# Optimization experiments

Measured on AMD Instinct MI355X. Metric: run time of the kernel, lower is better.

The kernel has to match this reference:

```python
import jax, jax.numpy as jnp
import numpy as np

N_NODES = 50000
N_EDGES = 640000
IN_C, HID_C, OUT_C = 64, 128, 64


def _glorot(key, fan_in, fan_out):
    lim = float(np.sqrt(6.0 / (fan_in + fan_out)))
    return jax.random.uniform(key, (fan_in, fan_out), jnp.float32, -lim, lim)


def setup_inputs() -> dict:
    key = jax.random.key(0)
    ks = jax.random.split(key, 16)
    x = jax.random.normal(ks[0], (N_NODES, IN_C), jnp.float32)
    edge_index = jax.random.randint(ks[1], (2, N_EDGES), 0, N_NODES, jnp.int64)
    # SAGEConv params: out = mean_aggr(x_j) @ Wl + x @ Wr + b
    dims = [(IN_C, HID_C), (HID_C, HID_C), (HID_C, OUT_C)]
    params = {}
    for i, (fi, fo) in enumerate(dims):
        params[f"Wl{i}"] = _glorot(ks[2 + 3 * i], fi, fo)
        params[f"Wr{i}"] = _glorot(ks[3 + 3 * i], fi, fo)
        params[f"b{i}"] = jnp.zeros((fo,), jnp.float32)
    # classifier: Linear(64,32) -> ReLU -> Linear(32,1) -> Sigmoid (dropout off in eval)
    params["Wc1"] = _glorot(ks[11], OUT_C, 32)
    params["bc1"] = jnp.zeros((32,), jnp.float32)
    params["Wc2"] = _glorot(ks[12], 32, 1)
    params["bc2"] = jnp.zeros((1,), jnp.float32)
    return {"x": x, "edge_index": edge_index, **params}


def _sage_conv(x, src, dst, Wl, Wr, b):
    # gather neighbor (source) features along edges, mean-aggregate at target
    msgs = x[src]                                                    # [E, C]
    agg = jax.ops.segment_sum(msgs, dst, num_segments=N_NODES)      # [N, C]
    deg = jax.ops.segment_sum(jnp.ones((src.shape[0], 1), x.dtype), dst,
                              num_segments=N_NODES)                 # [N, 1]
    agg = agg / jnp.maximum(deg, 1.0)
    return agg @ Wl + x @ Wr + b


def reference(x, edge_index, Wl0, Wr0, b0, Wl1, Wr1, b1, Wl2, Wr2, b2,
              Wc1, bc1, Wc2, bc2):
    src, dst = edge_index[0], edge_index[1]
    h = jax.nn.relu(_sage_conv(x, src, dst, Wl0, Wr0, b0))
    h = jax.nn.relu(_sage_conv(h, src, dst, Wl1, Wr1, b1))
    h = _sage_conv(h, src, dst, Wl2, Wr2, b2)                       # [N, 64]
    h = jax.nn.relu(h @ Wc1 + bc1)                                  # [N, 32]
    return jax.nn.sigmoid(h @ Wc2 + bc2)                            # [N, 1]
```

## Files before the change

kernel.cpp:

```cpp
#include <hip/hip_runtime.h>
#include <hip/hip_cooperative_groups.h>
#include <math.h>

namespace cg = cooperative_groups;

#define NN 50000
#define NE 640000
#define CAP 64

typedef short short8 __attribute__((ext_vector_type(8)));
typedef float f32x4  __attribute__((ext_vector_type(4)));

__device__ __forceinline__ unsigned bfr(float f) {
    unsigned u = __float_as_uint(f);
    return (u + 0x7FFFu + ((u >> 16) & 1u)) >> 16;
}
__device__ __forceinline__ unsigned pk2(float a, float b) { return bfr(a) | (bfr(b) << 16); }
__device__ __forceinline__ float bflo(unsigned u) { return __uint_as_float(u << 16); }
__device__ __forceinline__ float bfhi(unsigned u) { return __uint_as_float(u & 0xFFFF0000u); }

__device__ __forceinline__ void packOne(const float* Wl, const float* Wr,
                                        unsigned short* wp, int idx,
                                        int CIN, int COUT) {
    int k = idx / COUT, n = idx % COUT;
    float v = (k < CIN) ? Wl[k * COUT + n] : Wr[(k - CIN) * COUT + n];
    int kt = k >> 5, quad = (k >> 3) & 3, j = k & 7;
    int nt = n >> 4, l16 = n & 15;
    int NT = COUT / 16;
    wp[(((kt * NT + nt) * 64) + quad * 16 + l16) * 8 + j] = (unsigned short)bfr(v);
}

template <int LOGC>
__device__ __forceinline__ void
agg_phase(const unsigned* __restrict__ xu, const int* __restrict__ nbr,
          const int* __restrict__ cnt, unsigned* __restrict__ aggu,
          int gid, int ngroups, int l16) {
    constexpr int RU = 1 << (LOGC - 1);
    constexpr int PC = RU / 16;

    for (int gw = gid; gw < NN; gw += ngroups) {
        const int deg = cnt[gw];
        const int m = (deg < CAP) ? deg : CAP;

        float a[2 * PC] = {};

        for (int base = 0; base < m; base += 16) {
            int idx = NN;
            if (base + l16 < m) idx = nbr[gw * CAP + base + l16];
#pragma unroll
            for (int j = 0; j < 16; ++j) {
                const int n = __shfl(idx, j, 16);
                if (PC == 2) {
                    const uint2 u = *(const uint2*)(xu + (size_t)n * RU + l16 * 2);
                    a[0] += bflo(u.x); a[1] += bfhi(u.x);
                    a[2] += bflo(u.y); a[3] += bfhi(u.y);
                } else {
                    const uint4 u = *(const uint4*)(xu + (size_t)n * RU + l16 * 4);
                    a[0] += bflo(u.x); a[1] += bfhi(u.x);
                    a[2] += bflo(u.y); a[3] += bfhi(u.y);
                    a[4] += bflo(u.z); a[5] += bfhi(u.z);
                    a[6] += bflo(u.w); a[7] += bfhi(u.w);
                }
            }
        }

        const float di = 1.0f / (float)((deg > 1) ? deg : 1);
        if (PC == 2) {
            uint2 o = make_uint2(pk2(a[0] * di, a[1] * di), pk2(a[2] * di, a[3] * di));
            *(uint2*)(aggu + (size_t)gw * RU + l16 * 2) = o;
        } else {
            uint4 o = make_uint4(pk2(a[0] * di, a[1] * di), pk2(a[2] * di, a[3] * di),
                                 pk2(a[4] * di, a[5] * di), pk2(a[6] * di, a[7] * di));
            *(uint4*)(aggu + (size_t)gw * RU + l16 * 4) = o;
        }
    }
}

template <int CIN, int COUT, bool RELU>
__device__ __forceinline__ void
mfma_phase(const unsigned short* __restrict__ Agg, const unsigned short* __restrict__ X,
           const unsigned short* __restrict__ Wpack, const float* __restrict__ bias,
           unsigned short* __restrict__ outp, int blk, int gstride, int wave, int lane) {
    constexpr int KT = (2 * CIN) / 32;
    constexpr int NT = COUT / 16;
    const int quad = lane >> 4, l16 = lane & 15;
    const int NTILE = (NN + 127) / 128;

    for (int tile = blk; tile < NTILE; tile += gstride) {
        const int row_base = tile * 128 + wave * 32;
        int r0 = row_base + l16;      if (r0 >= NN) r0 = NN - 1;
        int r1 = row_base + 16 + l16; if (r1 >= NN) r1 = NN - 1;

        f32x4 acc[2][NT] = {};

        for (int kt = 0; kt < KT; ++kt) {
            const unsigned short* P = (kt < KT / 2) ? Agg : X;
            const int kb = (kt < KT / 2) ? kt * 32 : kt * 32 - CIN;
            const short8 a0 = *(const short8*)(P + (size_t)r0 * CIN + kb + quad * 8);
            const short8 a1 = *(const short8*)(P + (size_t)r1 * CIN + kb + quad * 8);
#pragma unroll
            for (int nt = 0; nt < NT; ++nt) {
                const short8 bfrag = *(const short8*)(Wpack + (size_t)((kt * NT + nt) * 64 + lane) * 8);
                acc[0][nt] = __builtin_amdgcn_mfma_f32_16x16x32_bf16(a0, bfrag, acc[0][nt], 0, 0, 0);
                acc[1][nt] = __builtin_amdgcn_mfma_f32_16x16x32_bf16(a1, bfrag, acc[1][nt], 0, 0, 0);
            }
        }

#pragma unroll
        for (int nt = 0; nt < NT; ++nt) {
            const int col = nt * 16 + l16;
            const float bb = bias[col];
#pragma unroll
            for (int s = 0; s < 2; ++s) {
#pragma unroll
                for (int rg = 0; rg < 4; ++rg) {
                    int row = row_base + s * 16 + quad * 4 + rg;
                    if (row < NN) {
                        float v = acc[s][nt][rg] + bb;
                        if (RELU) v = fmaxf(v, 0.f);
                        outp[(size_t)row * COUT + col] = (unsigned short)bfr(v);
                    }
                }
            }
        }
    }
}

__global__ __launch_bounds__(256) void
k_all(const int* __restrict__ src, const int* __restrict__ dst,
      const float* __restrict__ x,
      const float* Wl0, const float* Wr0, const float* b0,
      const float* Wl1, const float* Wr1, const float* b1,
      const float* Wl2, const float* Wr2, const float* b2,
      const float* Wc1, const float* bc1, const float* Wc2, const float* bc2,
      int* cnt, int* nbr, unsigned short* xb,
      unsigned short* wp0, unsigned short* wp1, unsigned short* wp2,
      unsigned short* wpc,
      unsigned short* aggb, unsigned short* h0b, unsigned short* h1b,
      float* out) {
    cg::grid_group grid = cg::this_grid();

    __shared__ __align__(16) short Hs[8 * 16 * 64];

    const int t = threadIdx.x, b = blockIdx.x;
    const int nthr = gridDim.x * 256;
    const int gt = b * 256 + t;
    const int wave = t >> 6, lane = t & 63;
    const int quad = lane >> 4, l16 = lane & 15;
    const int gid = gt >> 4;
    const int ngroups = nthr >> 4;

    for (int e = gt; e < NE; e += nthr) {
        int d = dst[e];
        int p = atomicAdd(&cnt[d], 1);
        if (p < CAP) nbr[d * CAP + p] = src[e];
    }
    for (int i = gt; i < NN * 16; i += nthr) {
        float4 v = ((const float4*)x)[i];
        ((uint2*)xb)[i] = make_uint2(pk2(v.x, v.y), pk2(v.z, v.w));
    }
    if (gt < 32) ((unsigned*)xb)[(size_t)NN * 32 + gt] = 0u;
    else if (gt < 96) ((unsigned*)h0b)[(size_t)NN * 64 + (gt - 32)] = 0u;
    else if (gt < 160) ((unsigned*)h1b)[(size_t)NN * 64 + (gt - 96)] = 0u;
    for (int i = gt; i < 67584; i += nthr) {
        if (i < 16384) packOne(Wl0, Wr0, wp0, i, 64, 128);
        else if (i < 49152) packOne(Wl1, Wr1, wp1, i - 16384, 128, 128);
        else if (i < 65536) packOne(Wl2, Wr2, wp2, i - 49152, 128, 64);
        else packOne(Wc1, Wc1, wpc, i - 65536, 64, 32);
    }
    grid.sync();

    agg_phase<6>((const unsigned*)xb, nbr, cnt, (unsigned*)aggb, gid, ngroups, t & 15);
    grid.sync();
    mfma_phase<64, 128, true>(aggb, xb, wp0, b0, h0b, b, gridDim.x, wave, lane);
    grid.sync();

    agg_phase<7>((const unsigned*)h0b, nbr, cnt, (unsigned*)aggb, gid, ngroups, t & 15);
    grid.sync();
    mfma_phase<128, 128, true>(aggb, h0b, wp1, b1, h1b, b, gridDim.x, wave, lane);
    grid.sync();

    agg_phase<7>((const unsigned*)h1b, nbr, cnt, (unsigned*)aggb, gid, ngroups, t & 15);
    grid.sync();

    {
        constexpr int CIN = 128, NT = 4, KT = 8;
        const int NTILE = (NN + 127) / 128;

        for (int tile = b; tile < NTILE; tile += gridDim.x) {
            const int row_base = tile * 128 + wave * 32;
            int r0 = row_base + l16;      if (r0 >= NN) r0 = NN - 1;
            int r1 = row_base + 16 + l16; if (r1 >= NN) r1 = NN - 1;

            f32x4 acc[2][NT] = {};

            for (int kt = 0; kt < KT; ++kt) {
                const unsigned short* P = (kt < KT / 2) ? aggb : h1b;
                const int kb = (kt < KT / 2) ? kt * 32 : kt * 32 - CIN;
                const short8 a0 = *(const short8*)(P + (size_t)r0 * CIN + kb + quad * 8);
                const short8 a1 = *(const short8*)(P + (size_t)r1 * CIN + kb + quad * 8);
#pragma unroll
                for (int nt = 0; nt < NT; ++nt) {
                    const short8 bfrag = *(const short8*)(wp2 + (size_t)((kt * NT + nt) * 64 + lane) * 8);
                    acc[0][nt] = __builtin_amdgcn_mfma_f32_16x16x32_bf16(a0, bfrag, acc[0][nt], 0, 0, 0);
                    acc[1][nt] = __builtin_amdgcn_mfma_f32_16x16x32_bf16(a1, bfrag, acc[1][nt], 0, 0, 0);
                }
            }

#pragma unroll
            for (int nt = 0; nt < NT; ++nt) {
                const float bb = b2[nt * 16 + l16];
#pragma unroll
                for (int s = 0; s < 2; ++s)
#pragma unroll
                    for (int rg = 0; rg < 4; ++rg)
                        Hs[(wave * 2 + s) * 1024 + (quad * 4 + rg) * 64 + nt * 16 + l16] =
                            (unsigned short)bfr(acc[s][nt][rg] + bb);
            }
            __syncthreads();

            f32x4 sacc[2][2] = {};
#pragma unroll
            for (int s = 0; s < 2; ++s)
#pragma unroll
                for (int kt2 = 0; kt2 < 2; ++kt2) {
                    const short8 af = *(const short8*)&Hs[(wave * 2 + s) * 1024 + l16 * 64 +
                                                          kt2 * 32 + quad * 8];
#pragma unroll
                    for (int nt2 = 0; nt2 < 2; ++nt2) {
                        const short8 bf = *(const short8*)(wpc + (size_t)((kt2 * 2 + nt2) * 64 + lane) * 8);
                        sacc[s][nt2] = __builtin_amdgcn_mfma_f32_16x16x32_bf16(af, bf, sacc[s][nt2], 0, 0, 0);
                    }
                }

            const float b1a = bc1[l16], b1b = bc1[16 + l16];
            const float w2a = Wc2[l16], w2b = Wc2[16 + l16];
            const float b2v = bc2[0];
#pragma unroll
            for (int s = 0; s < 2; ++s)
#pragma unroll
                for (int rg = 0; rg < 4; ++rg) {
                    float p = fmaxf(sacc[s][0][rg] + b1a, 0.f) * w2a +
                              fmaxf(sacc[s][1][rg] + b1b, 0.f) * w2b;
#pragma unroll
                    for (int off = 1; off < 16; off <<= 1) p += __shfl_xor(p, off);
                    if (l16 == 0) {
                        int row = row_base + s * 16 + quad * 4 + rg;
                        if (row < NN) out[row] = 1.0f / (1.0f + expf(-(p + b2v)));
                    }
                }
            __syncthreads();
        }
    }
}

__global__ __launch_bounds__(256) void
k_prep(const int* __restrict__ src, const int* __restrict__ dst,
       int* __restrict__ cnt, int* __restrict__ nbr,
       const float* __restrict__ x, unsigned* __restrict__ xb,
       const float* Wl0, const float* Wr0, const float* Wl1, const float* Wr1,
       const float* Wl2, const float* Wr2, const float* Wc1,
       unsigned short* wp0, unsigned short* wp1, unsigned short* wp2,
       unsigned short* wpc, unsigned short* h0b, unsigned short* h1b) {
    const int b = blockIdx.x, t = threadIdx.x;
    if (b < 2500) {
        int e = b * 256 + t;
        if (e < NE) {
            int d = dst[e];
            int p = atomicAdd(&cnt[d], 1);
            if (p < CAP) nbr[d * CAP + p] = src[e];
        }
        if (b == 0) {
            if (t < 32) xb[(size_t)NN * 32 + t] = 0u;
            else if (t < 96) ((unsigned*)h0b)[(size_t)NN * 64 + (t - 32)] = 0u;
            else if (t < 160) ((unsigned*)h1b)[(size_t)NN * 64 + (t - 96)] = 0u;
        }
    } else if (b < 5625) {
        int i = (b - 2500) * 256 + t;
        if (i < NN * 16) {
            float4 v = ((const float4*)x)[i];
            ((uint2*)xb)[i] = make_uint2(pk2(v.x, v.y), pk2(v.z, v.w));
        }
    } else {
        int idx = (b - 5625) * 256 + t;
        if (idx < 16384) packOne(Wl0, Wr0, wp0, idx, 64, 128);
        else if (idx < 49152) packOne(Wl1, Wr1, wp1, idx - 16384, 128, 128);
        else if (idx < 65536) packOne(Wl2, Wr2, wp2, idx - 49152, 128, 64);
        else if (idx < 67584) packOne(Wc1, Wc1, wpc, idx - 65536, 64, 32);
    }
}

template <int LOGC>
__global__ __launch_bounds__(256) void
k_aggregate(const unsigned* __restrict__ xu, const int* __restrict__ nbr,
            const int* __restrict__ cnt, unsigned* __restrict__ aggu, int N) {
    const int gid = (blockIdx.x * 256 + threadIdx.x) >> 4;
    if (gid >= N) return;
    agg_phase<LOGC>(xu, nbr, cnt, aggu, gid, 1 << 30, threadIdx.x & 15);
}

template <int CIN, int COUT, bool RELU>
__global__ __launch_bounds__(256) void
k_mfma(const unsigned short* __restrict__ Agg, const unsigned short* __restrict__ X,
       const unsigned short* __restrict__ Wpack, const float* __restrict__ bias,
       unsigned short* __restrict__ outp, int N) {
    mfma_phase<CIN, COUT, RELU>(Agg, X, Wpack, bias, outp,
                                blockIdx.x, 1 << 30, threadIdx.x >> 6, threadIdx.x & 63);
}

__global__ __launch_bounds__(256) void
k_mfma_cls(const unsigned short* __restrict__ Agg, const unsigned short* __restrict__ X,
           const unsigned short* __restrict__ Wpack, const unsigned short* __restrict__ WpackC,
           const float* __restrict__ bias, const float* __restrict__ bc1,
           const float* __restrict__ Wc2, const float* __restrict__ bc2,
           float* __restrict__ out, int N) {
    constexpr int CIN = 128, NT = 4, KT = 8;

    __shared__ __align__(16) short Hs[8 * 16 * 64];

    const int t = threadIdx.x;
    const int wave = t >> 6, lane = t & 63;
    const int quad = lane >> 4, l16 = lane & 15;

    const int row_base = blockIdx.x * 128 + wave * 32;
    int r0 = row_base + l16;      if (r0 >= N) r0 = N - 1;
    int r1 = row_base + 16 + l16; if (r1 >= N) r1 = N - 1;

    f32x4 acc[2][NT] = {};

    for (int kt = 0; kt < KT; ++kt) {
        const unsigned short* P = (kt < KT / 2) ? Agg : X;
        const int kb = (kt < KT / 2) ? kt * 32 : kt * 32 - CIN;
        const short8 a0 = *(const short8*)(P + (size_t)r0 * CIN + kb + quad * 8);
        const short8 a1 = *(const short8*)(P + (size_t)r1 * CIN + kb + quad * 8);
#pragma unroll
        for (int nt = 0; nt < NT; ++nt) {
            const short8 bfrag = *(const short8*)(Wpack + (size_t)((kt * NT + nt) * 64 + lane) * 8);
            acc[0][nt] = __builtin_amdgcn_mfma_f32_16x16x32_bf16(a0, bfrag, acc[0][nt], 0, 0, 0);
            acc[1][nt] = __builtin_amdgcn_mfma_f32_16x16x32_bf16(a1, bfrag, acc[1][nt], 0, 0, 0);
        }
    }

#pragma unroll
    for (int nt = 0; nt < NT; ++nt) {
        const float bb = bias[nt * 16 + l16];
#pragma unroll
        for (int s = 0; s < 2; ++s)
#pragma unroll
            for (int rg = 0; rg < 4; ++rg)
                Hs[(wave * 2 + s) * 1024 + (quad * 4 + rg) * 64 + nt * 16 + l16] =
                    (unsigned short)bfr(acc[s][nt][rg] + bb);
    }
    __syncthreads();

    f32x4 sacc[2][2] = {};
#pragma unroll
    for (int s = 0; s < 2; ++s)
#pragma unroll
        for (int kt2 = 0; kt2 < 2; ++kt2) {
            const short8 af = *(const short8*)&Hs[(wave * 2 + s) * 1024 + l16 * 64 +
                                                  kt2 * 32 + quad * 8];
#pragma unroll
            for (int nt2 = 0; nt2 < 2; ++nt2) {
                const short8 bf = *(const short8*)(WpackC + (size_t)((kt2 * 2 + nt2) * 64 + lane) * 8);
                sacc[s][nt2] = __builtin_amdgcn_mfma_f32_16x16x32_bf16(af, bf, sacc[s][nt2], 0, 0, 0);
            }
        }

    const float b1a = bc1[l16], b1b = bc1[16 + l16];
    const float w2a = Wc2[l16], w2b = Wc2[16 + l16];
    const float b2v = bc2[0];
#pragma unroll
    for (int s = 0; s < 2; ++s)
#pragma unroll
        for (int rg = 0; rg < 4; ++rg) {
            float p = fmaxf(sacc[s][0][rg] + b1a, 0.f) * w2a +
                      fmaxf(sacc[s][1][rg] + b1b, 0.f) * w2b;
#pragma unroll
            for (int off = 1; off < 16; off <<= 1) p += __shfl_xor(p, off);
            if (l16 == 0) {
                int row = row_base + s * 16 + quad * 4 + rg;
                if (row < N) out[row] = 1.0f / (1.0f + expf(-(p + b2v)));
            }
        }
}

extern "C" void kernel_launch(void* const* d_in, const int* in_sizes, int n_in,
                              void* d_out, int out_size, void* d_ws, size_t ws_size,
                              hipStream_t stream) {
    const float* x   = (const float*)d_in[0];
    const int*   ei  = (const int*)d_in[1];
    const int*   src = ei;
    const int*   dst = ei + NE;
    const float* Wl0 = (const float*)d_in[2];
    const float* Wr0 = (const float*)d_in[3];
    const float* b0  = (const float*)d_in[4];
    const float* Wl1 = (const float*)d_in[5];
    const float* Wr1 = (const float*)d_in[6];
    const float* b1  = (const float*)d_in[7];
    const float* Wl2 = (const float*)d_in[8];
    const float* Wr2 = (const float*)d_in[9];
    const float* b2  = (const float*)d_in[10];
    const float* Wc1 = (const float*)d_in[11];
    const float* bc1 = (const float*)d_in[12];
    const float* Wc2 = (const float*)d_in[13];
    const float* bc2 = (const float*)d_in[14];
    float* out = (float*)d_out;

    char*  ws   = (char*)d_ws;
    int*   cnt  = (int*)(ws);
    unsigned short* wp0 = (unsigned short*)(ws + (size_t)256 * 1024);
    unsigned short* wp1 = (unsigned short*)(ws + (size_t)352 * 1024);
    unsigned short* wp2 = (unsigned short*)(ws + (size_t)448 * 1024);
    unsigned short* wpc = (unsigned short*)(ws + (size_t)512 * 1024);
    int*   nbr  = (int*)(ws + (size_t)1 * (1 << 20));
    unsigned short* xb   = (unsigned short*)(ws + (size_t)16 * (1 << 20));
    unsigned short* aggb = (unsigned short*)(ws + (size_t)24 * (1 << 20));
    unsigned short* h0b  = (unsigned short*)(ws + (size_t)40 * (1 << 20));
    unsigned short* h1b  = (unsigned short*)(ws + (size_t)56 * (1 << 20));

    hipMemsetAsync(cnt, 0, (size_t)NN * sizeof(int), stream);

    bool coop_ok = false;
    int maxBpc = 0, ncu = 0, dev = 0;
    hipGetDevice(&dev);
    hipDeviceGetAttribute(&ncu, hipDeviceAttributeMultiprocessorCount, dev);
    hipError_t qerr = hipOccupancyMaxActiveBlocksPerMultiprocessor(
        &maxBpc, (const void*)k_all, 256, 0);
    if (qerr == hipSuccess && maxBpc > 0 && ncu > 0) {
        int grid = maxBpc * ncu;
        if (grid > 2048) grid = 2048;
        const int* srcp = src; const int* dstp = dst;
        void* args[] = {
            (void*)&srcp, (void*)&dstp, (void*)&x,
            (void*)&Wl0, (void*)&Wr0, (void*)&b0,
            (void*)&Wl1, (void*)&Wr1, (void*)&b1,
            (void*)&Wl2, (void*)&Wr2, (void*)&b2,
            (void*)&Wc1, (void*)&bc1, (void*)&Wc2, (void*)&bc2,
            (void*)&cnt, (void*)&nbr, (void*)&xb,
            (void*)&wp0, (void*)&wp1, (void*)&wp2, (void*)&wpc,
            (void*)&aggb, (void*)&h0b, (void*)&h1b,
            (void*)&out
        };
        hipError_t lerr = hipLaunchCooperativeKernel((const void*)k_all, dim3(grid),
                                                     dim3(256), args, 0, stream);
        if (lerr == hipSuccess) coop_ok = true;
        else (void)hipGetLastError();
    } else {
        (void)hipGetLastError();
    }

    if (!coop_ok) {
        const int B = 256;
        const int AGG_GRID = (NN * 16 + 255) / 256;
        const int MFMA_GRID = (NN + 127) / 128;

        k_prep<<<5889, B, 0, stream>>>(src, dst, cnt, nbr, x, (unsigned*)xb,
                                       Wl0, Wr0, Wl1, Wr1, Wl2, Wr2, Wc1,
                                       wp0, wp1, wp2, wpc, h0b, h1b);

        k_aggregate<6><<<AGG_GRID, B, 0, stream>>>((const unsigned*)xb, nbr, cnt,
                                                   (unsigned*)aggb, NN);
        k_mfma<64, 128, true><<<MFMA_GRID, B, 0, stream>>>(aggb, xb, wp0, b0, h0b, NN);

        k_aggregate<7><<<AGG_GRID, B, 0, stream>>>((const unsigned*)h0b, nbr, cnt,
                                                   (unsigned*)aggb, NN);
        k_mfma<128, 128, true><<<MFMA_GRID, B, 0, stream>>>(aggb, h0b, wp1, b1, h1b, NN);

        k_aggregate<7><<<AGG_GRID, B, 0, stream>>>((const unsigned*)h1b, nbr, cnt,
                                                   (unsigned*)aggb, NN);
        k_mfma_cls<<<MFMA_GRID, B, 0, stream>>>(aggb, h1b, wp2, wpc, b2, bc1, Wc2, bc2,
                                                out, NN);
    }
}
```

Before: 239.1 us.

## Fuse neighbor aggregation with MFMA linear per tile through LDS

Each layer's mean aggregation now runs per 64-row tile, writing the averaged features into shared memory. The MFMA matmul for that tile reads them straight back, which removes the global aggb round trip and half of the grid-wide barriers. The launch bounds add a minimum of 3 blocks per SM to hold occupancy. In exchange, the aggregation and MFMA work now alternate inside each block with __syncthreads between them, and tiles shrink from 128 to 64 rows.

Measured after the change: 676.8 us. 2.83x slower.

```diff
diff --git a/kernel.cpp b/kernel.cpp
--- a/kernel.cpp
+++ b/kernel.cpp
@@ -28,6 +28,202 @@
     int nt = n >> 4, l16 = n & 15;
     int NT = COUT / 16;
     wp[(((kt * NT + nt) * 64) + quad * 16 + l16) * 8 + j] = (unsigned short)bfr(v);
+}
+
+template <int CIN, int COUT, bool RELU, bool CLS>
+__device__ __forceinline__ void
+fused_layer(const unsigned* __restrict__ Fu, const unsigned short* __restrict__ Fs,
+            const int* __restrict__ nbr, const int* __restrict__ cnt,
+            const unsigned short* __restrict__ Wpack, const float* __restrict__ bias,
+            unsigned short* __restrict__ outp,
+            const unsigned short* __restrict__ WpackC, const float* __restrict__ bc1,
+            const float* __restrict__ Wc2, const float* __restrict__ bc2,
+            float* __restrict__ outf,
+            short* __restrict__ lds, int blk, int gstride, int t) {
+    constexpr int RU = CIN / 2;
+    constexpr int PC = RU / 16;
+    constexpr int RS = CIN + 8;
+    constexpr int KT = (2 * CIN) / 32;
+    constexpr int NT = COUT / 16;
+    const int NTILE = (NN + 63) / 64;
+
+    const int g = t >> 4, lg = t & 15;
+    const int wave = t >> 6, lane = t & 63;
+    const int quad = lane >> 4, l16 = lane & 15;
+
+    for (int tile = blk; tile < NTILE; tile += gstride) {
+#pragma unroll
+        for (int i = 0; i < 4; ++i) {
+            const int rloc = g * 4 + i;
+            const int gw = tile * 64 + rloc;
+            if (gw < NN) {
+                const int deg = cnt[gw];
+                const int m = (deg < CAP) ? deg : CAP;
+                float a[2 * PC] = {};
+                for (int base = 0; base < m; base += 16) {
+                    int idx = NN;
+                    if (base + lg < m) idx = nbr[gw * CAP + base + lg];
+#pragma unroll
+                    for (int j = 0; j < 16; ++j) {
+                        const int n = __shfl(idx, j, 16);
+                        if (PC == 2) {
+                            const uint2 u = *(const uint2*)(Fu + (size_t)n * RU + lg * 2);
+                            a[0] += bflo(u.x); a[1] += bfhi(u.x);
+                            a[2] += bflo(u.y); a[3] += bfhi(u.y);
+                        } else {
+                            const uint4 u = *(const uint4*)(Fu + (size_t)n * RU + lg * 4);
+                            a[0] += bflo(u.x); a[1] += bfhi(u.x);
+                            a[2] += bflo(u.y); a[3] += bfhi(u.y);
+                            a[4] += bflo(u.z); a[5] += bfhi(u.z);
+                            a[6] += bflo(u.w); a[7] += bfhi(u.w);
+                        }
+                    }
+                }
+                const float di = 1.0f / (float)((deg > 1) ? deg : 1);
+                unsigned* lrow = (unsigned*)lds + (size_t)rloc * (RU + 4) + lg * PC;
+                if (PC == 2)
+                    *(uint2*)lrow = make_uint2(pk2(a[0] * di, a[1] * di),
+                                               pk2(a[2] * di, a[3] * di));
+                else
+                    *(uint4*)lrow = make_uint4(pk2(a[0] * di, a[1] * di),
+                                               pk2(a[2] * di, a[3] * di),
+                                               pk2(a[4] * di, a[5] * di),
+                                               pk2(a[6] * di, a[7] * di));
+            }
+        }
+        __syncthreads();
+
+        const int rbase = tile * 64 + wave * 16;
+        int r0 = rbase + l16; if (r0 >= NN) r0 = NN - 1;
+        const int rloc0 = wave * 16 + l16;
+
+        f32x4 acc[NT] = {};
+#pragma unroll
+        for (int kt = 0; kt < KT; ++kt) {
+            short8 a0;
+            if (kt < KT / 2)
+                a0 = *(const short8*)(lds + (size_t)rloc0 * RS + kt * 32 + quad * 8);
+            else
+                a0 = *(const short8*)(Fs + (size_t)r0 * CIN + (kt * 32 - CIN) + quad * 8);
+#pragma unroll
+            for (int nt = 0; nt < NT; ++nt) {
+                const short8 bfrag = *(const short8*)(Wpack + (size_t)((kt * NT + nt) * 64 + lane) * 8);
+                acc[nt] = __builtin_amdgcn_mfma_f32_16x16x32_bf16(a0, bfrag, acc[nt], 0, 0, 0);
+            }
+        }
+
+        if constexpr (!CLS) {
+#pragma unroll
+            for (int nt = 0; nt < NT; ++nt) {
+                const float bb = bias[nt * 16 + l16];
+#pragma unroll
+                for (int rg = 0; rg < 4; ++rg) {
+                    const int row = rbase + quad * 4 + rg;
+                    if (row < NN) {
+                        float v = acc[nt][rg] + bb;
+                        if (RELU) v = fmaxf(v, 0.f);
+                        outp[(size_t)row * COUT + nt * 16 + l16] = (unsigned short)bfr(v);
+                    }
+                }
+            }
+            __syncthreads();
+        } else {
+            __syncthreads();
+            short* Hs = lds;
+#pragma unroll
+            for (int nt = 0; nt < NT; ++nt) {
+                const float bb = bias[nt * 16 + l16];
+#pragma unroll
+                for (int rg = 0; rg < 4; ++rg)
+                    Hs[wave * 1024 + (quad * 4 + rg) * 64 + nt * 16 + l16] =
+                        (short)(unsigned short)bfr(acc[nt][rg] + bb);
+            }
+            __syncthreads();
+
+            f32x4 sacc[2] = {};
+#pragma unroll
+            for (int kt2 = 0; kt2 < 2; ++kt2) {
+                const short8 af = *(const short8*)&Hs[wave * 1024 + l16 * 64 + kt2 * 32 + quad * 8];
+#pragma unroll
+                for (int nt2 = 0; nt2 < 2; ++nt2) {
+                    const short8 bf = *(const short8*)(WpackC + (size_t)((kt2 * 2 + nt2) * 64 + lane) * 8);
+                    sacc[nt2] = __builtin_amdgcn_mfma_f32_16x16x32_bf16(af, bf, sacc[nt2], 0, 0, 0);
+                }
+            }
+
+            const float b1a = bc1[l16], b1b = bc1[16 + l16];
+            const float w2a = Wc2[l16], w2b = Wc2[16 + l16];
+            const float b2v = bc2[0];
+#pragma unroll
+            for (int rg = 0; rg < 4; ++rg) {
+                float p = fmaxf(sacc[0][rg] + b1a, 0.f) * w2a +
+                          fmaxf(sacc[1][rg] + b1b, 0.f) * w2b;
+#pragma unroll
+                for (int off = 1; off < 16; off <<= 1) p += __shfl_xor(p, off);
+                if (l16 == 0) {
+                    const int row = rbase + quad * 4 + rg;
+                    if (row < NN) outf[row] = 1.0f / (1.0f + expf(-(p + b2v)));
+                }
+            }
+            __syncthreads();
+        }
+    }
+}
+
+__global__ __launch_bounds__(256, 3) void
+k_all(const int* __restrict__ src, const int* __restrict__ dst,
+      const float* __restrict__ x,
+      const float* Wl0, const float* Wr0, const float* b0,
+      const float* Wl1, const float* Wr1, const float* b1,
+      const float* Wl2, const float* Wr2, const float* b2,
+      const float* Wc1, const float* bc1, const float* Wc2, const float* bc2,
+      int* cnt, int* nbr, unsigned short* xb,
+      unsigned short* wp0, unsigned short* wp1, unsigned short* wp2,
+      unsigned short* wpc,
+      unsigned short* aggb, unsigned short* h0b, unsigned short* h1b,
+      float* out) {
+    cg::grid_group grid = cg::this_grid();
+    (void)aggb;
+
+    __shared__ __align__(16) short lds[64 * 136];
+
+    const int t = threadIdx.x, b = blockIdx.x;
+    const int nthr = gridDim.x * 256;
+    const int gt = b * 256 + t;
+
+    for (int e = gt; e < NE; e += nthr) {
+        int d = dst[e];
+        int p = atomicAdd(&cnt[d], 1);
+        if (p < CAP) nbr[d * CAP + p] = src[e];
+    }
+    for (int i = gt; i < NN * 16; i += nthr) {
+        float4 v = ((const float4*)x)[i];
+        ((uint2*)xb)[i] = make_uint2(pk2(v.x, v.y), pk2(v.z, v.w));
+    }
+    if (gt < 32) ((unsigned*)xb)[(size_t)NN * 32 + gt] = 0u;
+    else if (gt < 96) ((unsigned*)h0b)[(size_t)NN * 64 + (gt - 32)] = 0u;
+    else if (gt < 160) ((unsigned*)h1b)[(size_t)NN * 64 + (gt - 96)] = 0u;
+    for (int i = gt; i < 67584; i += nthr) {
+        if (i < 16384) packOne(Wl0, Wr0, wp0, i, 64, 128);
+        else if (i < 49152) packOne(Wl1, Wr1, wp1, i - 16384, 128, 128);
+        else if (i < 65536) packOne(Wl2, Wr2, wp2, i - 49152, 128, 64);
+        else packOne(Wc1, Wc1, wpc, i - 65536, 64, 32);
+    }
+    grid.sync();
+
+    fused_layer<64, 128, true, false>((const unsigned*)xb, xb, nbr, cnt, wp0, b0, h0b,
+                                      nullptr, nullptr, nullptr, nullptr, nullptr,
+                                      lds, b, gridDim.x, t);
+    grid.sync();
+
+    fused_layer<128, 128, true, false>((const unsigned*)h0b, h0b, nbr, cnt, wp1, b1, h1b,
+                                       nullptr, nullptr, nullptr, nullptr, nullptr,
+                                       lds, b, gridDim.x, t);
+    grid.sync();
+
+    fused_layer<128, 64, false, true>((const unsigned*)h1b, h1b, nbr, cnt, wp2, b2, nullptr,
+                                      wpc, bc1, Wc2, bc2, out,
+                                      lds, b, gridDim.x, t);
 }
 
 template <int LOGC>
@@ -122,134 +318,6 @@
                     }
                 }
             }
-        }
-    }
-}
-
-__global__ __launch_bounds__(256) void
-k_all(const int* __restrict__ src, const int* __restrict__ dst,
-      const float* __restrict__ x,
-      const float* Wl0, const float* Wr0, const float* b0,
-      const float* Wl1, const float* Wr1, const float* b1,
-      const float* Wl2, const float* Wr2, const float* b2,
-      const float* Wc1, const float* bc1, const float* Wc2, const float* bc2,
-      int* cnt, int* nbr, unsigned short* xb,
-      unsigned short* wp0, unsigned short* wp1, unsigned short* wp2,
-      unsigned short* wpc,
-      unsigned short* aggb, unsigned short* h0b, unsigned short* h1b,
-      float* out) {
-    cg::grid_group grid = cg::this_grid();
-
-    __shared__ __align__(16) short Hs[8 * 16 * 64];
-
-    const int t = threadIdx.x, b = blockIdx.x;
-    const int nthr = gridDim.x * 256;
-    const int gt = b * 256 + t;
-    const int wave = t >> 6, lane = t & 63;
-    const int quad = lane >> 4, l16 = lane & 15;
-    const int gid = gt >> 4;
-    const int ngroups = nthr >> 4;
-
-    for (int e = gt; e < NE; e += nthr) {
-        int d = dst[e];
-        int p = atomicAdd(&cnt[d], 1);
-        if (p < CAP) nbr[d * CAP + p] = src[e];
-    }
-    for (int i = gt; i < NN * 16; i += nthr) {
-        float4 v = ((const float4*)x)[i];
-        ((uint2*)xb)[i] = make_uint2(pk2(v.x, v.y), pk2(v.z, v.w));
-    }
-    if (gt < 32) ((unsigned*)xb)[(size_t)NN * 32 + gt] = 0u;
-    else if (gt < 96) ((unsigned*)h0b)[(size_t)NN * 64 + (gt - 32)] = 0u;
-    else if (gt < 160) ((unsigned*)h1b)[(size_t)NN * 64 + (gt - 96)] = 0u;
-    for (int i = gt; i < 67584; i += nthr) {
-        if (i < 16384) packOne(Wl0, Wr0, wp0, i, 64, 128);
-        else if (i < 49152) packOne(Wl1, Wr1, wp1, i - 16384, 128, 128);
-        else if (i < 65536) packOne(Wl2, Wr2, wp2, i - 49152, 128, 64);
-        else packOne(Wc1, Wc1, wpc, i - 65536, 64, 32);
-    }
-    grid.sync();
-
-    agg_phase<6>((const unsigned*)xb, nbr, cnt, (unsigned*)aggb, gid, ngroups, t & 15);
-    grid.sync();
-    mfma_phase<64, 128, true>(aggb, xb, wp0, b0, h0b, b, gridDim.x, wave, lane);
-    grid.sync();
-
-    agg_phase<7>((const unsigned*)h0b, nbr, cnt, (unsigned*)aggb, gid, ngroups, t & 15);
-    grid.sync();
-    mfma_phase<128, 128, true>(aggb, h0b, wp1, b1, h1b, b, gridDim.x, wave, lane);
-    grid.sync();
-
-    agg_phase<7>((const unsigned*)h1b, nbr, cnt, (unsigned*)aggb, gid, ngroups, t & 15);
-    grid.sync();
-
-    {
-        constexpr int CIN = 128, NT = 4, KT = 8;
-        const int NTILE = (NN + 127) / 128;
-
-        for (int tile = b; tile < NTILE; tile += gridDim.x) {
-            const int row_base = tile * 128 + wave * 32;
-            int r0 = row_base + l16;      if (r0 >= NN) r0 = NN - 1;
-            int r1 = row_base + 16 + l16; if (r1 >= NN) r1 = NN - 1;
-
-            f32x4 acc[2][NT] = {};
-
-            for (int kt = 0; kt < KT; ++kt) {
-                const unsigned short* P = (kt < KT / 2) ? aggb : h1b;
-                const int kb = (kt < KT / 2) ? kt * 32 : kt * 32 - CIN;
-                const short8 a0 = *(const short8*)(P + (size_t)r0 * CIN + kb + quad * 8);
-                const short8 a1 = *(const short8*)(P + (size_t)r1 * CIN + kb + quad * 8);
-#pragma unroll
-                for (int nt = 0; nt < NT; ++nt) {
-                    const short8 bfrag = *(const short8*)(wp2 + (size_t)((kt * NT + nt) * 64 + lane) * 8);
-                    acc[0][nt] = __builtin_amdgcn_mfma_f32_16x16x32_bf16(a0, bfrag, acc[0][nt], 0, 0, 0);
-                    acc[1][nt] = __builtin_amdgcn_mfma_f32_16x16x32_bf16(a1, bfrag, acc[1][nt], 0, 0, 0);
-                }
-            }
-
-#pragma unroll
-            for (int nt = 0; nt < NT; ++nt) {
-                const float bb = b2[nt * 16 + l16];
-#pragma unroll
-                for (int s = 0; s < 2; ++s)
-#pragma unroll
-                    for (int rg = 0; rg < 4; ++rg)
-                        Hs[(wave * 2 + s) * 1024 + (quad * 4 + rg) * 64 + nt * 16 + l16] =
-                            (unsigned short)bfr(acc[s][nt][rg] + bb);
-            }
-            __syncthreads();
-
-            f32x4 sacc[2][2] = {};
-#pragma unroll
-            for (int s = 0; s < 2; ++s)
-#pragma unroll
-                for (int kt2 = 0; kt2 < 2; ++kt2) {
-                    const short8 af = *(const short8*)&Hs[(wave * 2 + s) * 1024 + l16 * 64 +
-                                                          kt2 * 32 + quad * 8];
-#pragma unroll
-                    for (int nt2 = 0; nt2 < 2; ++nt2) {
-                        const short8 bf = *(const short8*)(wpc + (size_t)((kt2 * 2 + nt2) * 64 + lane) * 8);
-                        sacc[s][nt2] = __builtin_amdgcn_mfma_f32_16x16x32_bf16(af, bf, sacc[s][nt2], 0, 0, 0);
-                    }
-                }
-
-            const float b1a = bc1[l16], b1b = bc1[16 + l16];
-            const float w2a = Wc2[l16], w2b = Wc2[16 + l16];
-            const float b2v = bc2[0];
-#pragma unroll
-            for (int s = 0; s < 2; ++s)
-#pragma unroll
-                for (int rg = 0; rg < 4; ++rg) {
-                    float p = fmaxf(sacc[s][0][rg] + b1a, 0.f) * w2a +
-                              fmaxf(sacc[s][1][rg] + b1b, 0.f) * w2b;
-#pragma unroll
-                    for (int off = 1; off < 16; off <<= 1) p += __shfl_xor(p, off);
-                    if (l16 == 0) {
-                        int row = row_base + s * 16 + quad * 4 + rg;
-                        if (row < NN) out[row] = 1.0f / (1.0f + expf(-(p + b2v)));
-                    }
-                }
-            __syncthreads();
         }
     }
 }
```
